# Performance work log

Measured on AMD Instinct MI355X. Metric: run time of the kernel, lower is better.

The kernel has to match this reference:

```python
import jax, jax.numpy as jnp
import numpy as np

NUM_POPS = 8
K_ACTIVE = 2
IN, OUT = 2048, 2048
BATCH = 8192


def setup_inputs() -> dict:
    key = jax.random.key(0)
    ks = jax.random.split(key, 5)
    scale_in = 1.0 / np.sqrt(IN)
    return {
        "x": jax.random.normal(ks[0], (BATCH, IN), dtype=jnp.float32),
        # expert (population) linear params, stacked: W[p] is [OUT, IN]
        "W": jax.random.uniform(ks[1], (NUM_POPS, OUT, IN), dtype=jnp.float32, minval=-scale_in, maxval=scale_in),
        "b": jax.random.uniform(ks[2], (NUM_POPS, OUT), dtype=jnp.float32, minval=-scale_in, maxval=scale_in),
        # selector linear params
        "Ws": jax.random.uniform(ks[3], (NUM_POPS, IN), dtype=jnp.float32, minval=-scale_in, maxval=scale_in),
        "bs": jax.random.uniform(ks[4], (NUM_POPS,), dtype=jnp.float32, minval=-scale_in, maxval=scale_in),
    }


def reference(x, W, b, Ws, bs):
    # Eval-path math of SimplifiedDRNLayer: per-sample top-k expert selection,
    # uniform mean over the k selected experts' linear outputs.
    logits = x @ Ws.T + bs                      # [B, P]
    probs = jax.nn.softmax(logits, axis=-1)     # [B, P]
    _, topk_idx = jax.lax.top_k(probs, K_ACTIVE)  # [B, k] int32
    # combine weights: 1/k on selected experts, 0 elsewhere
    mask = jax.nn.one_hot(topk_idx, NUM_POPS, dtype=x.dtype).sum(axis=1) / K_ACTIVE  # [B, P]
    # all-expert outputs (P is small/fixed); [B, P, OUT]
    ys = jnp.einsum("poi,bi->bpo", W, x) + b
    out = jnp.einsum("bp,bpo->bo", mask, ys)    # [B, OUT]
    return out
```

## Files before the change

kernel.cpp:

```cpp
#include <hip/hip_runtime.h>
#include <stdint.h>

#define B_ROWS 8192
#define K_DIM 2048
#define N_DIM 2048
#define NPOP 8

typedef float f32x4 __attribute__((ext_vector_type(4)));
typedef __bf16 bf16x8 __attribute__((ext_vector_type(8)));

__device__ __forceinline__ unsigned short f2bf(float f) {
  unsigned int u = __float_as_uint(f);
  u += 0x7fffu + ((u >> 16) & 1u);
  return (unsigned short)(u >> 16);
}

__device__ __forceinline__ void glds16(const unsigned short* g, unsigned short* l) {
  __builtin_amdgcn_global_load_lds(
      (__attribute__((address_space(1))) unsigned int*)g,
      (__attribute__((address_space(3))) unsigned int*)l, 16, 0, 0);
}

__global__ void prep_w_kernel(const float* __restrict__ W, unsigned short* __restrict__ Wb) {
  const int n4 = NPOP * N_DIM * K_DIM / 4;
  int stride = gridDim.x * blockDim.x;
  for (int i = blockIdx.x * blockDim.x + threadIdx.x; i < n4; i += stride) {
    float4 v = reinterpret_cast<const float4*>(W)[i];
    ushort4 s;
    s.x = f2bf(v.x); s.y = f2bf(v.y); s.z = f2bf(v.z); s.w = f2bf(v.w);
    reinterpret_cast<ushort4*>(Wb)[i] = s;
  }
}

__global__ void prep_x_sel_kernel(const float* __restrict__ x,
                                  const float* __restrict__ Ws,
                                  const float* __restrict__ bs,
                                  unsigned short* __restrict__ xb,
                                  int* __restrict__ sel) {
  const int w = threadIdx.x >> 6;
  const int l = threadIdx.x & 63;
  const int r = blockIdx.x * 4 + w;

  float acc[NPOP];
#pragma unroll
  for (int p = 0; p < NPOP; ++p) acc[p] = 0.f;

  const float4* x4  = reinterpret_cast<const float4*>(x);
  const float4* Ws4 = reinterpret_cast<const float4*>(Ws);
#pragma unroll
  for (int j = 0; j < 8; ++j) {
    int idx = j * 256 + l * 4;
    float4 v = x4[(r * K_DIM + idx) >> 2];
    ushort4 s; s.x = f2bf(v.x); s.y = f2bf(v.y); s.z = f2bf(v.z); s.w = f2bf(v.w);
    *reinterpret_cast<ushort4*>(xb + (size_t)r * K_DIM + idx) = s;
#pragma unroll
    for (int p = 0; p < NPOP; ++p) {
      float4 wv = Ws4[(p * K_DIM + idx) >> 2];
      acc[p] += v.x * wv.x + v.y * wv.y + v.z * wv.z + v.w * wv.w;
    }
  }
#pragma unroll
  for (int off = 32; off > 0; off >>= 1)
#pragma unroll
    for (int p = 0; p < NPOP; ++p) acc[p] += __shfl_xor(acc[p], off, 64);

  if (l == 0) {
    float lg[NPOP];
#pragma unroll
    for (int p = 0; p < NPOP; ++p) lg[p] = acc[p] + bs[p];
    int p1 = 0;
#pragma unroll
    for (int p = 1; p < NPOP; ++p) if (lg[p] > lg[p1]) p1 = p;
    int p2 = -1;
#pragma unroll
    for (int p = 0; p < NPOP; ++p) {
      if (p == p1) continue;
      if (p2 < 0 || lg[p] > lg[p2]) p2 = p;
    }
    sel[r] = p1 * 8 + p2;
  }
}

__global__ __launch_bounds__(256) void build_lists_kernel(const int* __restrict__ sel,
                                                          int* __restrict__ lists,
                                                          int* __restrict__ cnt) {
  const int lid  = blockIdx.x;
  const int slot = lid >> 3;
  const int ex   = lid & 7;
  const int t    = threadIdx.x;

  __shared__ int psum[256];

  int local[32];
  int c = 0;
#pragma unroll
  for (int i = 0; i < 32; ++i) {
    int r = i * 256 + t;
    int s = sel[r];
    int e = slot ? (s & 7) : (s >> 3);
    if (e == ex) local[c++] = r;
  }
  psum[t] = c;
  __syncthreads();
  for (int off = 1; off < 256; off <<= 1) {
    int v = (t >= off) ? psum[t - off] : 0;
    __syncthreads();
    psum[t] += v;
    __syncthreads();
  }
  int start = psum[t] - c;
  for (int i = 0; i < c; ++i) lists[lid * 2048 + start + i] = local[i];
  if (t == 255) cnt[lid] = psum[255];
}


#define BAR()  asm volatile("s_barrier" ::: "memory")
#define VMW6   asm volatile("s_waitcnt vmcnt(6)" ::: "memory")
#define VMW0   asm volatile("s_waitcnt vmcnt(0)" ::: "memory")
#define SP(x)  __builtin_amdgcn_s_setprio(x)
#define SB0()  __builtin_amdgcn_sched_barrier(0)

#define STAGE_A(buf, msel, kt) do {                                            \
    unsigned short* lb_ = &As[buf][(msel) * 8192 + w * 512];                   \
    glds16((const unsigned short*)((const char*)xb + (aoff##msel##0 + (unsigned)((kt) * 128))), lb_); \
    glds16((const unsigned short*)((const char*)xb + (aoff##msel##1 + (unsigned)((kt) * 128))), lb_ + 4096); \
  } while (0)

#define STAGE_B(buf, nsel, kt) do {                                            \
    unsigned short* lb_ = &Bs[buf][(nsel) * 8192 + w * 512];                   \
    glds16((const unsigned short*)((const char*)wgp + (boff##nsel##0 + (unsigned)((kt) * 128))), lb_); \
    glds16((const unsigned short*)((const char*)wgp + (boff##nsel##1 + (unsigned)((kt) * 128))), lb_ + 4096); \
  } while (0)

#define LOAD_AF(buf, msel) do {                                                \
    const char* ab_ = (const char*)&As[0][0] + (buf) * 32768 + (msel) * 16384 + arow_rd; \
    _Pragma("unroll") for (int mi_ = 0; mi_ < 4; ++mi_) {                      \
      af[mi_][0] = *(const bf16x8*)(ab_ + mi_ * 2048 + csw0);                  \
      af[mi_][1] = *(const bf16x8*)(ab_ + mi_ * 2048 + csw1); }                \
  } while (0)

#define LOAD_BF(dst, buf, nsel) do {                                           \
    const char* bb_ = (const char*)&Bs[0][0] + (buf) * 32768 + (nsel) * 16384 + brow_rd; \
    _Pragma("unroll") for (int ni_ = 0; ni_ < 2; ++ni_) {                      \
      dst[ni_][0] = *(const bf16x8*)(bb_ + ni_ * 2048 + csw0);                 \
      dst[ni_][1] = *(const bf16x8*)(bb_ + ni_ * 2048 + csw1); }               \
  } while (0)

#define MMA(msel, nsel, bfv) do {                                              \
    _Pragma("unroll") for (int mi_ = 0; mi_ < 4; ++mi_)                        \
    _Pragma("unroll") for (int ni_ = 0; ni_ < 2; ++ni_) {                      \
      f32x4 a_ = acc[(msel)*4+mi_][(nsel)*2+ni_];                              \
      a_ = __builtin_amdgcn_mfma_f32_16x16x32_bf16(af[mi_][0], bfv[ni_][0], a_, 0, 0, 0); \
      a_ = __builtin_amdgcn_mfma_f32_16x16x32_bf16(af[mi_][1], bfv[ni_][1], a_, 0, 0, 0); \
      acc[(msel)*4+mi_][(nsel)*2+ni_] = a_; }                                  \
  } while (0)

#define HALF_ITER(buf, obuf, kt, DO1, DO2, VM) do {                            \
    LOAD_AF(buf, 0); LOAD_BF(bf0, buf, 0);                                     \
    if (DO1) STAGE_B(obuf, 1, (kt) + 1);                                       \
    BAR(); SP(1); MMA(0, 0, bf0); SP(0); SB0(); BAR();                         \
    LOAD_BF(bf1, buf, 1);                                                      \
    if (DO2) STAGE_A(buf, 0, (kt) + 2);                                        \
    BAR(); SP(1); MMA(0, 1, bf1); SP(0); SB0(); BAR();                         \
    LOAD_AF(buf, 1);                                                           \
    if (DO2) STAGE_B(buf, 0, (kt) + 2);                                        \
    BAR(); SP(1); MMA(1, 1, bf1); SP(0); SB0(); BAR();                         \
    if (DO2) STAGE_A(buf, 1, (kt) + 2);                                        \
    VM;                                                                        \
    BAR(); SP(1); MMA(1, 0, bf0); SP(0); SB0(); BAR();                         \
  } while (0)

#define EPILOGUE(STMT)                                                         \
  _Pragma("unroll") for (int mi8 = 0; mi8 < 8; ++mi8) {                        \
    const int rb = wm * 128 + ((mi8 >> 2) << 6) + ((mi8 & 3) << 4) + (quad << 2); \
    _Pragma("unroll") for (int j = 0; j < 4; ++j) {                            \
      int r = m0 + rb + j;                                                     \
      if (r < cg) {                                                            \
        int gr = list[r];                                                      \
        float* orow = out + (size_t)gr * N_DIM + n0 + wn * 64;                 \
        _Pragma("unroll") for (int nj = 0; nj < 4; ++nj) {                     \
          int col = ((nj >> 1) << 5) + ((nj & 1) << 4) + lane16;               \
          float v = 0.5f * acc[mi8][nj][j] + 0.5f * bv[nj];                    \
          STMT;                                                                \
        } } } }

__global__ __launch_bounds__(512, 2) void gemm_kernel(
    const unsigned short* __restrict__ xb,
    const unsigned short* __restrict__ Wb,
    const float* __restrict__ bvec,
    const int* __restrict__ lists,
    const int* __restrict__ cnt,
    float* __restrict__ out,
    int pass) {
  const int bid = blockIdx.x;
  const int g   = bid & 7;
  const int mt  = (bid >> 3) & 7;
  const int nt  = bid >> 6;
  const int lid = pass * 8 + g;
  const int cg  = cnt[lid];
  const int m0  = mt * 256;
  if (m0 >= cg) return;
  const int n0 = nt * 256;

  __shared__ __align__(16) unsigned short As[2][16384];
  __shared__ __align__(16) unsigned short Bs[2][16384];

  const int t = threadIdx.x;
  const int w = t >> 6, l = t & 63;
  const int lane16 = l & 15, quad = l >> 4;
  const int wm = w >> 2, wn = w & 3;
  const int l8 = l >> 3;
  const unsigned int swS = (unsigned)(((l & 7) ^ l8) << 4);
  const unsigned int swR = (unsigned)((l & 7) << 4);
  const unsigned int csw0 = ((unsigned)(quad << 4)) ^ swR;
  const unsigned int csw1 = ((unsigned)(64 | (quad << 4))) ^ swR;
  const unsigned int arow_rd = (unsigned)(wm * 8192 + lane16 * 128);
  const unsigned int brow_rd = (unsigned)(wn * 4096 + lane16 * 128);

  const int* list = lists + lid * 2048;
  const unsigned short* wgp = Wb + (size_t)g * (N_DIM * K_DIM);

  const int trb = w * 8 + l8;
  int r00 = m0 + trb;        int g00 = (r00 < cg) ? list[r00] : 0;
  int r01 = m0 + 128 + trb;  int g01 = (r01 < cg) ? list[r01] : 0;
  int r10 = m0 + 64 + trb;   int g10 = (r10 < cg) ? list[r10] : 0;
  int r11 = m0 + 192 + trb;  int g11 = (r11 < cg) ? list[r11] : 0;
  const unsigned int aoff00 = (unsigned)g00 * 4096u + swS;
  const unsigned int aoff01 = (unsigned)g01 * 4096u + swS;
  const unsigned int aoff10 = (unsigned)g10 * 4096u + swS;
  const unsigned int aoff11 = (unsigned)g11 * 4096u + swS;
  const int rl0 = w * 8 + l8, rl1 = 64 + w * 8 + l8;
  const int b0 = n0 + ((rl0 >> 5) << 6) + (rl0 & 31);
  const int b1 = n0 + ((rl1 >> 5) << 6) + (rl1 & 31);
  const unsigned int boff00 = (unsigned)b0 * 4096u + swS;
  const unsigned int boff01 = (unsigned)b1 * 4096u + swS;
  const unsigned int boff10 = boff00 + 32u * 4096u;
  const unsigned int boff11 = boff01 + 32u * 4096u;

  bf16x8 af[4][2], bf0[2][2], bf1[2][2];
  f32x4 acc[8][4];
#pragma unroll
  for (int i = 0; i < 8; ++i)
#pragma unroll
    for (int jq = 0; jq < 4; ++jq) { f32x4 z = {0.f, 0.f, 0.f, 0.f}; acc[i][jq] = z; }

  STAGE_A(0, 0, 0); STAGE_B(0, 0, 0); STAGE_A(0, 1, 0); STAGE_B(0, 1, 0);
  STAGE_A(1, 0, 1); STAGE_B(1, 0, 1); STAGE_A(1, 1, 1);
  VMW6;
  BAR();

#pragma unroll 1
  for (int h = 0; h < 30; h += 2) {
    HALF_ITER(0, 1, h,     1, 1, VMW6);
    HALF_ITER(1, 0, h + 1, 1, 1, VMW6);
  }
  HALF_ITER(0, 1, 30, 1, 0, VMW0);
  HALF_ITER(1, 0, 31, 0, 0, (void)0);

  const float* bias = bvec + (size_t)g * N_DIM + n0 + wn * 64;
  float bv[4];
#pragma unroll
  for (int nj = 0; nj < 4; ++nj) bv[nj] = bias[((nj >> 1) << 5) + ((nj & 1) << 4) + lane16];

  if (pass == 0) { EPILOGUE(orow[col] = v); }
  else           { EPILOGUE(orow[col] += v); }
}

extern "C" void kernel_launch(void* const* d_in, const int* in_sizes, int n_in,
                              void* d_out, int out_size, void* d_ws, size_t ws_size,
                              hipStream_t stream) {
  const float* x  = (const float*)d_in[0];
  const float* W  = (const float*)d_in[1];
  const float* b  = (const float*)d_in[2];
  const float* Ws = (const float*)d_in[3];
  const float* bs = (const float*)d_in[4];
  float* out = (float*)d_out;

  char* ws = (char*)d_ws;
  unsigned short* Wb = (unsigned short*)ws;
  unsigned short* xb = (unsigned short*)(ws + (size_t)67108864);
  int* lists = (int*)(ws + (size_t)67108864 + 33554432);
  int* cnt   = (int*)(ws + (size_t)67108864 + 33554432 + 131072);
  int* sel   = (int*)(ws + (size_t)67108864 + 33554432 + 131072 + 4096);

  prep_w_kernel<<<4096, 256, 0, stream>>>(W, Wb);
  prep_x_sel_kernel<<<2048, 256, 0, stream>>>(x, Ws, bs, xb, sel);
  build_lists_kernel<<<16, 256, 0, stream>>>(sel, lists, cnt);
  gemm_kernel<<<dim3(512), dim3(512), 0, stream>>>(xb, Wb, b, lists, cnt, out, 0);
  gemm_kernel<<<dim3(512), dim3(512), 0, stream>>>(xb, Wb, b, lists, cnt, out, 1);
}
```

Before: 546.5 us.

## Merge two grouped-GEMM passes into one launch with atomic-add epilogue

Both top-k slots are now processed by a single GEMM launch of twice as many blocks. The output is zeroed inside the x-prep kernel, and every block accumulates its result into it with atomic float adds. This removes the second launch and the serial dependency between the passes, and fills the GPU better. The B-tile staging is also moved so both B halves for the current buffer are issued together, with the wait count raised to match. The cost is an extra full write of the output to zero it, atomic traffic in the epilogue, and summation order that is no longer fixed.

```diff
diff --git a/kernel.cpp b/kernel.cpp
--- a/kernel.cpp
+++ b/kernel.cpp
@@ -36,7 +36,16 @@
                                   const float* __restrict__ Ws,
                                   const float* __restrict__ bs,
                                   unsigned short* __restrict__ xb,
-                                  int* __restrict__ sel) {
+                                  int* __restrict__ sel,
+                                  float* __restrict__ out) {
+  {
+    float4 z4 = {0.f, 0.f, 0.f, 0.f};
+    float4* o4 = reinterpret_cast<float4*>(out);
+    const int n4 = B_ROWS * N_DIM / 4;
+    int stride = gridDim.x * blockDim.x;
+    for (int i = blockIdx.x * blockDim.x + threadIdx.x; i < n4; i += stride) o4[i] = z4;
+  }
+
   const int w = threadIdx.x >> 6;
   const int l = threadIdx.x & 63;
   const int r = blockIdx.x * 4 + w;
@@ -115,7 +124,7 @@
 
 
 #define BAR()  asm volatile("s_barrier" ::: "memory")
-#define VMW6   asm volatile("s_waitcnt vmcnt(6)" ::: "memory")
+#define VMW8   asm volatile("s_waitcnt vmcnt(8)" ::: "memory")
 #define VMW0   asm volatile("s_waitcnt vmcnt(0)" ::: "memory")
 #define SP(x)  __builtin_amdgcn_s_setprio(x)
 #define SB0()  __builtin_amdgcn_sched_barrier(0)
@@ -155,22 +164,21 @@
       acc[(msel)*4+mi_][(nsel)*2+ni_] = a_; }                                  \
   } while (0)
 
-#define HALF_ITER(buf, obuf, kt, DO1, DO2, VM) do {                            \
+#define HALF_ITER(buf, kt, DOS, VM) do {                                       \
     LOAD_AF(buf, 0); LOAD_BF(bf0, buf, 0);                                     \
-    if (DO1) STAGE_B(obuf, 1, (kt) + 1);                                       \
     BAR(); SP(1); MMA(0, 0, bf0); SP(0); SB0(); BAR();                         \
     LOAD_BF(bf1, buf, 1);                                                      \
-    if (DO2) STAGE_A(buf, 0, (kt) + 2);                                        \
+    if (DOS) STAGE_A(buf, 0, (kt) + 2);                                        \
     BAR(); SP(1); MMA(0, 1, bf1); SP(0); SB0(); BAR();                         \
     LOAD_AF(buf, 1);                                                           \
-    if (DO2) STAGE_B(buf, 0, (kt) + 2);                                        \
+    if (DOS) { STAGE_B(buf, 0, (kt) + 2); STAGE_B(buf, 1, (kt) + 2); }         \
     BAR(); SP(1); MMA(1, 1, bf1); SP(0); SB0(); BAR();                         \
-    if (DO2) STAGE_A(buf, 1, (kt) + 2);                                        \
+    if (DOS) STAGE_A(buf, 1, (kt) + 2);                                        \
     VM;                                                                        \
     BAR(); SP(1); MMA(1, 0, bf0); SP(0); SB0(); BAR();                         \
   } while (0)
 
-#define EPILOGUE(STMT)                                                         \
+#define EPILOGUE()                                                             \
   _Pragma("unroll") for (int mi8 = 0; mi8 < 8; ++mi8) {                        \
     const int rb = wm * 128 + ((mi8 >> 2) << 6) + ((mi8 & 3) << 4) + (quad << 2); \
     _Pragma("unroll") for (int j = 0; j < 4; ++j) {                            \
@@ -181,7 +189,7 @@
         _Pragma("unroll") for (int nj = 0; nj < 4; ++nj) {                     \
           int col = ((nj >> 1) << 5) + ((nj & 1) << 4) + lane16;               \
           float v = 0.5f * acc[mi8][nj][j] + 0.5f * bv[nj];                    \
-          STMT;                                                                \
+          (void)unsafeAtomicAdd(&orow[col], v);                                \
         } } } }
 
 __global__ __launch_bounds__(512, 2) void gemm_kernel(
@@ -190,15 +198,15 @@
     const float* __restrict__ bvec,
     const int* __restrict__ lists,
     const int* __restrict__ cnt,
-    float* __restrict__ out,
-    int pass) {
-  const int bid = blockIdx.x;
-  const int g   = bid & 7;
-  const int mt  = (bid >> 3) & 7;
-  const int nt  = bid >> 6;
-  const int lid = pass * 8 + g;
-  const int cg  = cnt[lid];
-  const int m0  = mt * 256;
+    float* __restrict__ out) {
+  const int bid  = blockIdx.x;
+  const int g    = bid & 7;
+  const int mt   = (bid >> 3) & 7;
+  const int slot = (bid >> 6) & 1;
+  const int nt   = bid >> 7;
+  const int lid  = slot * 8 + g;
+  const int cg   = cnt[lid];
+  const int m0   = mt * 256;
   if (m0 >= cg) return;
   const int n0 = nt * 256;
 
@@ -244,26 +252,25 @@
 #pragma unroll
     for (int jq = 0; jq < 4; ++jq) { f32x4 z = {0.f, 0.f, 0.f, 0.f}; acc[i][jq] = z; }
 
-  STAGE_A(0, 0, 0); STAGE_B(0, 0, 0); STAGE_A(0, 1, 0); STAGE_B(0, 1, 0);
-  STAGE_A(1, 0, 1); STAGE_B(1, 0, 1); STAGE_A(1, 1, 1);
-  VMW6;
+  STAGE_A(0, 0, 0); STAGE_B(0, 0, 0); STAGE_B(0, 1, 0); STAGE_A(0, 1, 0);
+  STAGE_A(1, 0, 1); STAGE_B(1, 0, 1); STAGE_B(1, 1, 1); STAGE_A(1, 1, 1);
+  VMW8;
   BAR();
 
 #pragma unroll 1
   for (int h = 0; h < 30; h += 2) {
-    HALF_ITER(0, 1, h,     1, 1, VMW6);
-    HALF_ITER(1, 0, h + 1, 1, 1, VMW6);
-  }
-  HALF_ITER(0, 1, 30, 1, 0, VMW0);
-  HALF_ITER(1, 0, 31, 0, 0, (void)0);
+    HALF_ITER(0, h,     1, VMW8);
+    HALF_ITER(1, h + 1, 1, VMW8);
+  }
+  HALF_ITER(0, 30, 0, VMW0);
+  HALF_ITER(1, 31, 0, (void)0);
 
   const float* bias = bvec + (size_t)g * N_DIM + n0 + wn * 64;
   float bv[4];
 #pragma unroll
   for (int nj = 0; nj < 4; ++nj) bv[nj] = bias[((nj >> 1) << 5) + ((nj & 1) << 4) + lane16];
 
-  if (pass == 0) { EPILOGUE(orow[col] = v); }
-  else           { EPILOGUE(orow[col] += v); }
+  EPILOGUE();
 }
 
 extern "C" void kernel_launch(void* const* d_in, const int* in_sizes, int n_in,
@@ -284,8 +291,7 @@
   int* sel   = (int*)(ws + (size_t)67108864 + 33554432 + 131072 + 4096);
 
   prep_w_kernel<<<4096, 256, 0, stream>>>(W, Wb);
-  prep_x_sel_kernel<<<2048, 256, 0, stream>>>(x, Ws, bs, xb, sel);
+  prep_x_sel_kernel<<<2048, 256, 0, stream>>>(x, Ws, bs, xb, sel, out);
   build_lists_kernel<<<16, 256, 0, stream>>>(sel, lists, cnt);
-  gemm_kernel<<<dim3(512), dim3(512), 0, stream>>>(xb, Wb, b, lists, cnt, out, 0);
-  gemm_kernel<<<dim3(512), dim3(512), 0, stream>>>(xb, Wb, b, lists, cnt, out, 1);
-}
+  gemm_kernel<<<dim3(1024), dim3(512), 0, stream>>>(xb, Wb, b, lists, cnt, out);
+}
```

Measured after the change: 574.3 us. 1.05x slower.
